# Performance work log

Hardware: AMD Instinct MI355X
Metric: run time of the kernel (lower is better)

## Reference

```python
import jax, jax.numpy as jnp
import numpy as np

N = 50000        # number of nodes
E = 1600000      # number of (directed) edges, ~degree 32
D = 128          # latent_dim
L = 2            # num_layers
NEG_SLOPE = 0.01 # torch F.leaky_relu default


def setup_inputs() -> dict:
    key = jax.random.key(0)
    k1, k2, k3, k4 = jax.random.split(key, 4)
    h = jax.random.normal(k1, (N, D), dtype=jnp.float32)
    src = jax.random.randint(k2, (E,), 0, N, dtype=jnp.int32)
    dst = jax.random.randint(k3, (E,), 0, N, dtype=jnp.int32)
    # attn_fc per layer: Linear(2*D, 1, bias=False) -> weight vector of length 2*D
    att_w = jax.random.normal(k4, (L, 2 * D), dtype=jnp.float32) * 0.1
    return {"h": h, "src": src, "dst": dst, "att_w": att_w}


def _segment_softmax(e, seg, n):
    # numerically-stable softmax over edges grouped by destination node
    m = jax.ops.segment_max(e, seg, num_segments=n)      # [N]
    ex = jnp.exp(e - m[seg])                             # [E]
    s = jax.ops.segment_sum(ex, seg, num_segments=n)     # [N]
    return ex / s[seg]


def reference(h, src, dst, att_w):
    n, d = h.shape
    for l in range(att_w.shape[0]):
        w_src = att_w[l, :d]   # weight applied to edges.src['h']
        w_dst = att_w[l, d:]   # weight applied to edges.dst['h']
        # a = attn_fc(concat(h_src, h_dst)) = h_src @ w_src + h_dst @ w_dst
        a = h[src] @ w_src + h[dst] @ w_dst               # [E]
        e = jnp.where(a > 0, a, NEG_SLOPE * a)            # leaky_relu
        alpha = _segment_softmax(e, dst, n)               # edge_softmax by dst
        # update_all: m = h_src * e ; h_dst = sum(m)
        h = jax.ops.segment_sum(h[src] * alpha[:, None], dst, num_segments=n)
    return h
```

## Files before the change

kernel.cpp:

```cpp
#include <hip/hip_runtime.h>
#include <hip/hip_fp16.h>
#include <math.h>

#define NEG_SLOPE 0.01f
#define BKT_BITS 7
#define BKT_MASK 127
#define SBLOCKS  128


__global__ void bkhist_kernel(const int* __restrict__ dst, int* __restrict__ blockhist,
                              int E, int NB, int chunk) {
    extern __shared__ int lh[];
    for (int k = threadIdx.x; k < NB; k += blockDim.x) lh[k] = 0;
    __syncthreads();
    int b = blockIdx.x;
    int beg = b * chunk, end = min(E, beg + chunk);
    for (int e = beg + (int)threadIdx.x; e < end; e += blockDim.x)
        atomicAdd(&lh[dst[e] >> BKT_BITS], 1);
    __syncthreads();
    for (int k = threadIdx.x; k < NB; k += blockDim.x)
        blockhist[k * SBLOCKS + b] = lh[k];
}

__global__ void scan1_kernel(const int* __restrict__ in, int* __restrict__ local_excl,
                             int* __restrict__ partials, int n) {
    __shared__ int sm[1024];
    int i = blockIdx.x * 1024 + threadIdx.x;
    int x = (i < n) ? in[i] : 0;
    sm[threadIdx.x] = x;
    __syncthreads();
    for (int off = 1; off < 1024; off <<= 1) {
        int y = (threadIdx.x >= (unsigned)off) ? sm[threadIdx.x - off] : 0;
        __syncthreads();
        sm[threadIdx.x] += y;
        __syncthreads();
    }
    if (i < n) local_excl[i] = sm[threadIdx.x] - x;
    if (threadIdx.x == 1023) partials[blockIdx.x] = sm[1023];
}

__global__ void scan2_kernel(int* __restrict__ partials, int nchunks) {
    __shared__ int sm[1024];
    int x = (threadIdx.x < (unsigned)nchunks) ? partials[threadIdx.x] : 0;
    sm[threadIdx.x] = x;
    __syncthreads();
    for (int off = 1; off < 1024; off <<= 1) {
        int y = (threadIdx.x >= (unsigned)off) ? sm[threadIdx.x - off] : 0;
        __syncthreads();
        sm[threadIdx.x] += y;
        __syncthreads();
    }
    partials[threadIdx.x] = sm[threadIdx.x] - x;
    if (threadIdx.x == 1023) partials[1024] = sm[1023];
}

__global__ void scan3_kernel(const int* __restrict__ local_excl, const int* __restrict__ partials,
                             int* __restrict__ out, int n) {
    int i = blockIdx.x * 1024 + threadIdx.x;
    if (i < n) out[i] = local_excl[i] + partials[blockIdx.x];
    if (i == n) out[n] = partials[1024];
}

__global__ void bksplit_kernel(const int* __restrict__ src, const int* __restrict__ dst,
                               const int* __restrict__ bh_scan, unsigned* __restrict__ pairs,
                               int E, int NB, int chunk) {
    extern __shared__ int lm[];
    int* lbase = lm;
    int* lcnt  = lm + NB;
    int b = blockIdx.x;
    for (int k = threadIdx.x; k < NB; k += blockDim.x) {
        lbase[k] = bh_scan[k * SBLOCKS + b];
        lcnt[k]  = 0;
    }
    __syncthreads();
    int beg = b * chunk, end = min(E, beg + chunk);
    for (int e = beg + (int)threadIdx.x; e < end; e += blockDim.x) {
        int d = dst[e];
        int k = d >> BKT_BITS;
        int pos = lbase[k] + atomicAdd(&lcnt[k], 1);
        pairs[pos] = ((unsigned)src[e] << BKT_BITS) | (unsigned)(d & BKT_MASK);
    }
}

__global__ void csr_build_kernel(const unsigned* __restrict__ pairs, const int* __restrict__ bh_scan,
                                 int* __restrict__ row_ptr, int* __restrict__ csr_src,
                                 int E, int N, int NB) {
    __shared__ int ldeg[128];
    __shared__ int lscan[128];
    __shared__ int lpos[128];
    int k = blockIdx.x;
    int bbase = bh_scan[k * SBLOCKS];
    int bend  = bh_scan[(k + 1) * SBLOCKS];
    if (threadIdx.x < 128) ldeg[threadIdx.x] = 0;
    __syncthreads();
    for (int i = bbase + (int)threadIdx.x; i < bend; i += blockDim.x)
        atomicAdd(&ldeg[pairs[i] & BKT_MASK], 1);
    __syncthreads();
    int x = (threadIdx.x < 128) ? ldeg[threadIdx.x] : 0;
    if (threadIdx.x < 128) lscan[threadIdx.x] = x;
    __syncthreads();
    for (int off = 1; off < 128; off <<= 1) {
        int y = 0;
        if (threadIdx.x < 128 && threadIdx.x >= (unsigned)off) y = lscan[threadIdx.x - off];
        __syncthreads();
        if (threadIdx.x < 128) lscan[threadIdx.x] += y;
        __syncthreads();
    }
    if (threadIdx.x < 128) {
        int excl = lscan[threadIdx.x] - x;
        int node = (k << BKT_BITS) + threadIdx.x;
        if (node < N) row_ptr[node] = bbase + excl;
        lpos[threadIdx.x] = excl;
    }
    if (k == NB - 1 && threadIdx.x == 0) row_ptr[N] = E;
    __syncthreads();
    for (int i = bbase + (int)threadIdx.x; i < bend; i += blockDim.x) {
        unsigned p = pairs[i];
        int pos = atomicAdd(&lpos[p & BKT_MASK], 1);
        csr_src[bbase + pos] = (int)(p >> BKT_BITS);
    }
}


__global__ void stconv_kernel(const float* __restrict__ h, const float* __restrict__ att_w_l,
                              float* __restrict__ s, float* __restrict__ t,
                              __half* __restrict__ h16, int n) {
    int gid  = blockIdx.x * blockDim.x + threadIdx.x;
    int v    = gid >> 6;
    int lane = threadIdx.x & 63;
    if (v >= n) return;
    float2 hv = ((const float2*)(h + (size_t)v * 128))[lane];
    ((__half2*)(h16 + (size_t)v * 128))[lane] = __floats2half2_rn(hv.x, hv.y);
    float2 ws = ((const float2*)att_w_l)[lane];
    float2 wd = ((const float2*)(att_w_l + 128))[lane];
    float ps = hv.x * ws.x + hv.y * ws.y;
    float pt = hv.x * wd.x + hv.y * wd.y;
    for (int off = 32; off > 0; off >>= 1) {
        ps += __shfl_down(ps, off);
        pt += __shfl_down(pt, off);
    }
    if (lane == 0) { s[v] = ps; t[v] = pt; }
}

template<bool LAST>
__global__ void agg_kernel(const __half* __restrict__ hin, const float* __restrict__ s,
                           const float* __restrict__ t, const int* __restrict__ row_ptr,
                           const int* __restrict__ csr_src,
                           __half* __restrict__ hout16, float* __restrict__ outf,
                           const float* __restrict__ att_w_next,
                           float* __restrict__ s2, float* __restrict__ t2, int n) {
    int gid   = blockIdx.x * blockDim.x + threadIdx.x;
    int v     = gid >> 6;
    int lane  = threadIdx.x & 63;
    if (v >= n) return;
    int half  = lane >> 5;
    int hlane = lane & 31;

    int beg = row_ptr[v];
    int end = row_ptr[v + 1];
    float tv = t[v];

    float4 acc = make_float4(0.f, 0.f, 0.f, 0.f);
    float lsum = 0.f;
    int i = beg;
    #define GATHER(uu, wgt)                                                    \
        { float2 r = ((const float2*)(hin + (size_t)(uu) * 128))[hlane];       \
          float2 f01 = __half22float2(*(const __half2*)&r.x);                  \
          float2 f23 = __half22float2(*(const __half2*)&r.y);                  \
          acc.x = fmaf(wgt, f01.x, acc.x); acc.y = fmaf(wgt, f01.y, acc.y);    \
          acc.z = fmaf(wgt, f23.x, acc.z); acc.w = fmaf(wgt, f23.y, acc.w); }
    for (; i + 7 < end; i += 8) {
        int u0 = csr_src[i     + half];
        int u1 = csr_src[i + 2 + half];
        int u2 = csr_src[i + 4 + half];
        int u3 = csr_src[i + 6 + half];
        float a0 = s[u0] + tv, a1 = s[u1] + tv, a2 = s[u2] + tv, a3 = s[u3] + tv;
        float e0 = (a0 > 0.f) ? a0 : NEG_SLOPE * a0;
        float e1 = (a1 > 0.f) ? a1 : NEG_SLOPE * a1;
        float e2 = (a2 > 0.f) ? a2 : NEG_SLOPE * a2;
        float e3 = (a3 > 0.f) ? a3 : NEG_SLOPE * a3;
        float w0 = __expf(e0), w1 = __expf(e1), w2 = __expf(e2), w3 = __expf(e3);
        lsum += (w0 + w1) + (w2 + w3);
        GATHER(u0, w0); GATHER(u1, w1); GATHER(u2, w2); GATHER(u3, w3);
    }
    for (; i + 1 < end; i += 2) {
        int u = csr_src[i + half];
        float a = s[u] + tv;
        float e = (a > 0.f) ? a : NEG_SLOPE * a;
        float wu = __expf(e);
        lsum += wu;
        GATHER(u, wu);
    }
    if (i < end) {
        int u = csr_src[i];
        float a = s[u] + tv;
        float e = (a > 0.f) ? a : NEG_SLOPE * a;
        float wu = (half == 0) ? __expf(e) : 0.f;
        lsum += wu;
        GATHER(u, wu);
    }
    #undef GATHER
    acc.x += __shfl_xor(acc.x, 32);
    acc.y += __shfl_xor(acc.y, 32);
    acc.z += __shfl_xor(acc.z, 32);
    acc.w += __shfl_xor(acc.w, 32);
    lsum  += __shfl_xor(lsum, 32);
    float inv_l = (lsum > 0.f) ? (1.0f / lsum) : 0.f;
    acc.x *= inv_l; acc.y *= inv_l; acc.z *= inv_l; acc.w *= inv_l;

    if (LAST) {
        if (half == 0)
            ((float4*)(outf + (size_t)v * 128))[hlane] = acc;
    } else {
        if (half == 0) {
            __half2 q01 = __floats2half2_rn(acc.x, acc.y);
            __half2 q23 = __floats2half2_rn(acc.z, acc.w);
            float2 packed;
            packed.x = *(const float*)&q01;
            packed.y = *(const float*)&q23;
            ((float2*)(hout16 + (size_t)v * 128))[hlane] = packed;
        }
        float4 ws4 = ((const float4*)att_w_next)[hlane];
        float4 wd4 = ((const float4*)(att_w_next + 128))[hlane];
        float ps = acc.x * ws4.x + acc.y * ws4.y + acc.z * ws4.z + acc.w * ws4.w;
        float pt = acc.x * wd4.x + acc.y * wd4.y + acc.z * wd4.z + acc.w * wd4.w;
        for (int off = 16; off > 0; off >>= 1) {
            ps += __shfl_down(ps, off);
            pt += __shfl_down(pt, off);
        }
        if (lane == 0) { s2[v] = ps; t2[v] = pt; }
    }
}


extern "C" void kernel_launch(void* const* d_in, const int* in_sizes, int n_in,
                              void* d_out, int out_size, void* d_ws, size_t ws_size,
                              hipStream_t stream) {
    const float* h0    = (const float*)d_in[0];
    const int*   src   = (const int*)d_in[1];
    const int*   dst   = (const int*)d_in[2];
    const float* att_w = (const float*)d_in[3];
    int N = in_sizes[0] / 128;
    int E = in_sizes[1];
    int L = in_sizes[3] / 256;
    float* out = (float*)d_out;

    int NB = (N + BKT_MASK) >> BKT_BITS;
    int n2 = NB * SBLOCKS;
    int chunk = (E + SBLOCKS - 1) / SBLOCKS;
    int nch2 = (n2 + 1023) / 1024;

    char* ws = (char*)d_ws;
    size_t off = 0;
    auto alloc = [&](size_t bytes) -> void* {
        void* p = ws + off;
        off = (off + bytes + 511) & ~(size_t)511;
        return p;
    };
    int*      row_ptr   = (int*)     alloc((size_t)(N + 1) * 4);
    int*      csr_src   = (int*)     alloc((size_t)E * 4);
    float*    s1        = (float*)   alloc((size_t)N * 4);
    float*    t1        = (float*)   alloc((size_t)N * 4);
    float*    s2        = (float*)   alloc((size_t)N * 4);
    float*    t2        = (float*)   alloc((size_t)N * 4);
    __half*   hA        = (__half*)  alloc((size_t)N * 128 * 2);
    __half*   hB        = (__half*)  alloc((size_t)N * 128 * 2);
    unsigned* pairs     = (unsigned*)alloc((size_t)E * 4);
    int*      blockhist = (int*)     alloc((size_t)n2 * 4);
    int*      bh_scan   = (int*)     alloc((size_t)(n2 + 1) * 4);
    int*      local_ex  = (int*)     alloc((size_t)n2 * 4);
    int*      partials  = (int*)     alloc(1025 * 4);

    bkhist_kernel<<<SBLOCKS, 256, NB * 4, stream>>>(dst, blockhist, E, NB, chunk);
    scan1_kernel<<<nch2, 1024, 0, stream>>>(blockhist, local_ex, partials, n2);
    scan2_kernel<<<1, 1024, 0, stream>>>(partials, nch2);
    scan3_kernel<<<nch2, 1024, 0, stream>>>(local_ex, partials, bh_scan, n2);
    bksplit_kernel<<<SBLOCKS, 256, 2 * NB * 4, stream>>>(src, dst, bh_scan, pairs, E, NB, chunk);
    csr_build_kernel<<<NB, 256, 0, stream>>>(pairs, bh_scan, row_ptr, csr_src, E, N, NB);

    const int tb = 256;
    int node_blocks = (N * 64 + tb - 1) / tb;

    stconv_kernel<<<node_blocks, tb, 0, stream>>>(h0, att_w, s1, t1, hA, N);

    __half* hin = hA;
    __half* hnx = hB;
    float *sc = s1, *tc = t1, *sn = s2, *tn = t2;
    for (int l = 0; l < L; ++l) {
        if (l == L - 1) {
            agg_kernel<true><<<node_blocks, tb, 0, stream>>>(
                hin, sc, tc, row_ptr, csr_src, nullptr, out, nullptr, nullptr, nullptr, N);
        } else {
            agg_kernel<false><<<node_blocks, tb, 0, stream>>>(
                hin, sc, tc, row_ptr, csr_src, hnx, nullptr,
                att_w + (size_t)(l + 1) * 256, sn, tn, N);
            __half* tmp = hin; hin = hnx; hnx = tmp;
            float* tf;
            tf = sc; sc = sn; sn = tf;
            tf = tc; tc = tn; tn = tf;
        }
    }
}
```

Baseline: 266.5 us.

## Cooperatively load edge indices and weights per wave, retune CSR build launches

The aggregation kernel now has all 64 lanes load up to 64 neighbor indices and compute their softmax weights in parallel. Each half-wave then gets its gather index and weight by shuffle, instead of every half-wave reloading csr_src and s[] and recomputing exp for each edge. Separately, the CSR-build kernels get more blocks and threads (SBLOCKS 256, 512 threads per block). This cuts redundant scalar loads and exp work, at the cost of extra shuffles and a full-wave reduction for the normaliser.

```diff
diff --git a/kernel.cpp b/kernel.cpp
--- a/kernel.cpp
+++ b/kernel.cpp
@@ -5,7 +5,8 @@
 #define NEG_SLOPE 0.01f
 #define BKT_BITS 7
 #define BKT_MASK 127
-#define SBLOCKS  128
+#define SBLOCKS  256
+#define STPB     512
 
 
 __global__ void bkhist_kernel(const int* __restrict__ dst, int* __restrict__ blockhist,
@@ -142,6 +143,15 @@
     if (lane == 0) { s[v] = ps; t[v] = pt; }
 }
 
+__device__ __forceinline__ void gath(const __half* __restrict__ hin, int uu, float wgt,
+                                     int hlane, float4& acc) {
+    float2 r = ((const float2*)(hin + (size_t)uu * 128))[hlane];
+    float2 f01 = __half22float2(*(const __half2*)&r.x);
+    float2 f23 = __half22float2(*(const __half2*)&r.y);
+    acc.x = fmaf(wgt, f01.x, acc.x); acc.y = fmaf(wgt, f01.y, acc.y);
+    acc.z = fmaf(wgt, f23.x, acc.z); acc.w = fmaf(wgt, f23.y, acc.w);
+}
+
 template<bool LAST>
 __global__ void agg_kernel(const __half* __restrict__ hin, const float* __restrict__ s,
                            const float* __restrict__ t, const int* __restrict__ row_ptr,
@@ -161,50 +171,42 @@
     float tv = t[v];
 
     float4 acc = make_float4(0.f, 0.f, 0.f, 0.f);
-    float lsum = 0.f;
-    int i = beg;
-    #define GATHER(uu, wgt)                                                    \
-        { float2 r = ((const float2*)(hin + (size_t)(uu) * 128))[hlane];       \
-          float2 f01 = __half22float2(*(const __half2*)&r.x);                  \
-          float2 f23 = __half22float2(*(const __half2*)&r.y);                  \
-          acc.x = fmaf(wgt, f01.x, acc.x); acc.y = fmaf(wgt, f01.y, acc.y);    \
-          acc.z = fmaf(wgt, f23.x, acc.z); acc.w = fmaf(wgt, f23.y, acc.w); }
-    for (; i + 7 < end; i += 8) {
-        int u0 = csr_src[i     + half];
-        int u1 = csr_src[i + 2 + half];
-        int u2 = csr_src[i + 4 + half];
-        int u3 = csr_src[i + 6 + half];
-        float a0 = s[u0] + tv, a1 = s[u1] + tv, a2 = s[u2] + tv, a3 = s[u3] + tv;
-        float e0 = (a0 > 0.f) ? a0 : NEG_SLOPE * a0;
-        float e1 = (a1 > 0.f) ? a1 : NEG_SLOPE * a1;
-        float e2 = (a2 > 0.f) ? a2 : NEG_SLOPE * a2;
-        float e3 = (a3 > 0.f) ? a3 : NEG_SLOPE * a3;
-        float w0 = __expf(e0), w1 = __expf(e1), w2 = __expf(e2), w3 = __expf(e3);
-        lsum += (w0 + w1) + (w2 + w3);
-        GATHER(u0, w0); GATHER(u1, w1); GATHER(u2, w2); GATHER(u3, w3);
-    }
-    for (; i + 1 < end; i += 2) {
-        int u = csr_src[i + half];
+    float lsum_l = 0.f;
+
+    for (int base = beg; base < end; base += 64) {
+        int cnt = end - base;
+        if (cnt > 64) cnt = 64;
+        int idx = base + min(lane, cnt - 1);
+        int u   = csr_src[idx];
         float a = s[u] + tv;
         float e = (a > 0.f) ? a : NEG_SLOPE * a;
-        float wu = __expf(e);
-        lsum += wu;
-        GATHER(u, wu);
-    }
-    if (i < end) {
-        int u = csr_src[i];
-        float a = s[u] + tv;
-        float e = (a > 0.f) ? a : NEG_SLOPE * a;
-        float wu = (half == 0) ? __expf(e) : 0.f;
-        lsum += wu;
-        GATHER(u, wu);
-    }
-    #undef GATHER
+        float wl = (lane < cnt) ? __expf(e) : 0.f;
+        lsum_l += wl;
+        int steps = (cnt + 1) >> 1;
+        int k = 0;
+        for (; k + 1 < steps; k += 2) {
+            int sl0 = (k << 1) + half;
+            int sl1 = (k << 1) + 2 + half;
+            int   u0 = __shfl(u, sl0);
+            float w0 = __shfl(wl, sl0);
+            int   u1 = __shfl(u, sl1);
+            float w1 = __shfl(wl, sl1);
+            gath(hin, u0, w0, hlane, acc);
+            gath(hin, u1, w1, hlane, acc);
+        }
+        if (k < steps) {
+            int sl = (k << 1) + half;
+            int   u0 = __shfl(u, sl);
+            float w0 = __shfl(wl, sl);
+            gath(hin, u0, w0, hlane, acc);
+        }
+    }
+    float lsum = lsum_l;
+    for (int off = 32; off > 0; off >>= 1) lsum += __shfl_xor(lsum, off);
     acc.x += __shfl_xor(acc.x, 32);
     acc.y += __shfl_xor(acc.y, 32);
     acc.z += __shfl_xor(acc.z, 32);
     acc.w += __shfl_xor(acc.w, 32);
-    lsum  += __shfl_xor(lsum, 32);
     float inv_l = (lsum > 0.f) ? (1.0f / lsum) : 0.f;
     acc.x *= inv_l; acc.y *= inv_l; acc.z *= inv_l; acc.w *= inv_l;
 
@@ -271,12 +273,12 @@
     int*      local_ex  = (int*)     alloc((size_t)n2 * 4);
     int*      partials  = (int*)     alloc(1025 * 4);
 
-    bkhist_kernel<<<SBLOCKS, 256, NB * 4, stream>>>(dst, blockhist, E, NB, chunk);
+    bkhist_kernel<<<SBLOCKS, STPB, NB * 4, stream>>>(dst, blockhist, E, NB, chunk);
     scan1_kernel<<<nch2, 1024, 0, stream>>>(blockhist, local_ex, partials, n2);
     scan2_kernel<<<1, 1024, 0, stream>>>(partials, nch2);
     scan3_kernel<<<nch2, 1024, 0, stream>>>(local_ex, partials, bh_scan, n2);
-    bksplit_kernel<<<SBLOCKS, 256, 2 * NB * 4, stream>>>(src, dst, bh_scan, pairs, E, NB, chunk);
-    csr_build_kernel<<<NB, 256, 0, stream>>>(pairs, bh_scan, row_ptr, csr_src, E, N, NB);
+    bksplit_kernel<<<SBLOCKS, STPB, 2 * NB * 4, stream>>>(src, dst, bh_scan, pairs, E, NB, chunk);
+    csr_build_kernel<<<NB, 512, 0, stream>>>(pairs, bh_scan, row_ptr, csr_src, E, N, NB);
 
     const int tb = 256;
     int node_blocks = (N * 64 + tb - 1) / tb;
```

New measurement: 238.2 us. 1.12x faster.
